# Performance work log

Hardware: AMD Instinct MI355X
Metric: run time of the kernel (lower is better)

## Reference

```python
import jax, jax.numpy as jnp
import numpy as np

N_NODES = 50000
N_EDGES = 1600000
DIM_IN = 64
DIM = 64
DIM_OUT = 32
N_GRAPHS = 64
DELTA = 2.5749
BN_EPS = 1e-5


def _lin(x, W, b):
    return x @ W.T + b


def _pna_conv(x, src, dst, mlp_W, mlp_b, W1, b1, W2, b2):
    # GINConv with overridden PNA aggregate: nn(x + aggr(x_j))
    msgs = x[src]                                               # [E, d]
    n = x.shape[0]
    sums = jax.ops.segment_sum(msgs, dst, num_segments=n)       # [N, d]
    maxs = jax.ops.segment_max(msgs, dst, num_segments=n)
    cnt = jax.ops.segment_sum(jnp.ones((msgs.shape[0], 1), msgs.dtype), dst,
                              num_segments=n)                   # [N, 1]
    means = sums / cnt
    var = jax.nn.relu(jax.ops.segment_sum(msgs * msgs, dst, num_segments=n) / cnt
                      - means * means)
    aggr = jnp.concatenate([sums, maxs, means, var], axis=1)    # [N, 4d]
    comb = jnp.concatenate([aggr, (cnt / DELTA) * aggr, (DELTA / cnt) * aggr],
                           axis=1)                              # [N, 12d]
    a = _lin(comb, mlp_W, mlp_b)                                # [N, d]
    h = x + a                                                   # (1+eps)*x + aggr, eps=0
    return _lin(jax.nn.relu(_lin(h, W1, b1)), W2, b2)


def _bn(x, g, b):
    # BatchNorm1d with batch statistics (training-mode stats, biased var)
    m = x.mean(axis=0)
    v = ((x - m) ** 2).mean(axis=0)
    return g * (x - m) / jnp.sqrt(v + BN_EPS) + b


def setup_inputs() -> dict:
    key = jax.random.key(0)
    ks = jax.random.split(key, 32)
    x = jax.random.normal(ks[0], (N_NODES, DIM_IN), dtype=jnp.float32)
    src = jax.random.randint(ks[1], (N_EDGES,), 0, N_NODES)
    dst = jax.random.randint(ks[2], (N_EDGES,), 0, N_NODES)
    # guarantee every node has >=1 incoming edge (original divides by bincount)
    dst = dst.at[:N_NODES].set(jnp.arange(N_NODES))
    edge_index = jnp.stack([src, dst]).astype(jnp.int32)
    batch = jnp.sort(jax.random.randint(ks[3], (N_NODES,), 0, N_GRAPHS)).astype(jnp.int32)

    def w(k, shape):
        return jax.random.normal(k, shape, dtype=jnp.float32) * 0.1

    d = {"x": x, "edge_index": edge_index, "batch": batch}
    i = 4
    for c in ("c1", "c2", "c3"):
        d[f"{c}_mlp_W"] = w(ks[i], (DIM, DIM * 12)); i += 1
        d[f"{c}_mlp_b"] = jnp.zeros((DIM,), jnp.float32)
        d[f"{c}_W1"] = w(ks[i], (DIM, DIM)); i += 1
        d[f"{c}_b1"] = jnp.zeros((DIM,), jnp.float32)
        d[f"{c}_W2"] = w(ks[i], (DIM, DIM)); i += 1
        d[f"{c}_b2"] = jnp.zeros((DIM,), jnp.float32)
    for b in ("bn1", "bn2", "bn3"):
        d[f"{b}_g"] = jnp.ones((DIM,), jnp.float32)
        d[f"{b}_b"] = jnp.zeros((DIM,), jnp.float32)
    d["fc1_W"] = w(ks[i], (DIM, DIM)); i += 1
    d["fc1_b"] = jnp.zeros((DIM,), jnp.float32)
    d["fc2_W"] = w(ks[i], (DIM_OUT, DIM)); i += 1
    d["fc2_b"] = jnp.zeros((DIM_OUT,), jnp.float32)
    return d


def reference(x, edge_index, batch,
              c1_mlp_W, c1_mlp_b, c1_W1, c1_b1, c1_W2, c1_b2, bn1_g, bn1_b,
              c2_mlp_W, c2_mlp_b, c2_W1, c2_b1, c2_W2, c2_b2, bn2_g, bn2_b,
              c3_mlp_W, c3_mlp_b, c3_W1, c3_b1, c3_W2, c3_b2, bn3_g, bn3_b,
              fc1_W, fc1_b, fc2_W, fc2_b):
    src, dst = edge_index[0], edge_index[1]
    h = jax.nn.relu(_pna_conv(x, src, dst, c1_mlp_W, c1_mlp_b, c1_W1, c1_b1, c1_W2, c1_b2))
    h = _bn(h, bn1_g, bn1_b)
    h = jax.nn.relu(_pna_conv(h, src, dst, c2_mlp_W, c2_mlp_b, c2_W1, c2_b1, c2_W2, c2_b2))
    h = _bn(h, bn2_g, bn2_b)
    h = jax.nn.relu(_pna_conv(h, src, dst, c3_mlp_W, c3_mlp_b, c3_W1, c3_b1, c3_W2, c3_b2))
    h = _bn(h, bn3_g, bn3_b)
    g = jax.ops.segment_sum(h, batch, num_segments=N_GRAPHS)   # global_add_pool
    g = jax.nn.relu(_lin(g, fc1_W, fc1_b))                     # dropout disabled (eval)
    g = _lin(g, fc2_W, fc2_b)
    return jax.nn.log_softmax(g, axis=-1)
```

## Files before the change

### kernel.cpp

```cpp
#include <hip/hip_runtime.h>

#define NN 50000
#define NE 1600000
#define DD 64
#define NGRAPH 64
#define DOUT 32
#define DELTA_F 2.5749f
#define BN_EPS_F 1e-5f

typedef unsigned short ushort;
typedef __attribute__((ext_vector_type(8))) short short8;
typedef __attribute__((ext_vector_type(4))) float floatx4;

static __device__ __forceinline__ float blo(unsigned u) {
    return __uint_as_float(u << 16);
}
static __device__ __forceinline__ float bhi(unsigned u) {
    return __uint_as_float(u & 0xFFFF0000u);
}
static __device__ __forceinline__ float bu2f(ushort u) {
    return __uint_as_float(((unsigned)u) << 16);
}
static __device__ __forceinline__ ushort f2bu(float f) {
    unsigned u = __float_as_uint(f);
    unsigned r = (u + 0x7FFF + ((u >> 16) & 1)) >> 16;
    return (ushort)r;
}
static __device__ __forceinline__ unsigned pk(float a, float b) {
    return ((unsigned)f2bu(b) << 16) | (unsigned)f2bu(a);
}

__global__ void k_prep(const float* __restrict__ x, ushort* __restrict__ XH,
                       const float* __restrict__ w0, const float* __restrict__ w1,
                       const float* __restrict__ w2,
                       const float* __restrict__ a0, const float* __restrict__ a1,
                       const float* __restrict__ a2, const float* __restrict__ a3,
                       const float* __restrict__ a4, const float* __restrict__ a5,
                       ushort* __restrict__ Wb, ushort* __restrict__ Wsb,
                       int* __restrict__ counts, float* __restrict__ bnstat,
                       float* __restrict__ gpool) {
    int i = blockIdx.x * 256 + threadIdx.x;
    if (i < NN) counts[i] = 0;
    if (i < 384) bnstat[i] = 0.f;
    if (i < NGRAPH * DD) gpool[i] = 0.f;
    if (i < NN * 16) {
        float4 v = *(const float4*)(x + (size_t)i * 4);
        ushort4 h;
        h.x = f2bu(v.x); h.y = f2bu(v.y); h.z = f2bu(v.z); h.w = f2bu(v.w);
        *(ushort4*)(XH + (size_t)i * 4) = h;
    }
    if (i < 3 * 65536) {
        int layer = i / 65536, r = i % 65536;
        const float* w = (layer == 0) ? w0 : ((layer == 1) ? w1 : w2);
        int c = r / 16384, r2 = r % 16384;
        int kb = r2 >> 11, r3 = r2 & 2047;
        int t = r3 >> 9, r4 = r3 & 511;
        int l = r4 >> 3, j = r4 & 7;
        int k = kb * 32 + (l >> 4) * 8 + j;
        int o = t * 16 + (l & 15);
        int g = (c == 0) ? 0 : ((c == 3) ? 2 : 1);
        float wv = w[o * 768 + g * 256 + k];
        ushort h = f2bu(wv);
        Wb[i] = (c == 2) ? f2bu(wv - bu2f(h)) : h;
    } else if (i < 3 * 65536 + 3 * 16384) {
        int i2 = i - 3 * 65536;
        int layer = i2 / 16384, r = i2 % 16384;
        int lin = r >> 13, r2 = r & 8191;
        int hl = r2 >> 12, r3 = r2 & 4095;
        int kb = r3 >> 11, r4 = r3 & 2047;
        int t = r4 >> 9, r5 = r4 & 511;
        int l = r5 >> 3, j = r5 & 7;
        int k = kb * 32 + (l >> 4) * 8 + j;
        int o = t * 16 + (l & 15);
        const float* w = (lin == 0)
            ? ((layer == 0) ? a0 : (layer == 1) ? a2 : a4)
            : ((layer == 0) ? a1 : (layer == 1) ? a3 : a5);
        float wv = w[o * 64 + k];
        ushort h = f2bu(wv);
        Wsb[i2] = hl ? f2bu(wv - bu2f(h)) : h;
    }
}

__global__ void k_rank(const int* __restrict__ dst, int* __restrict__ counts,
                       int* __restrict__ rank) {
    int i = blockIdx.x * 256 + threadIdx.x;
    if (i < NE / 4) {
        int4 d = ((const int4*)dst)[i];
        int4 r;
        r.x = atomicAdd(&counts[d.x], 1);
        r.y = atomicAdd(&counts[d.y], 1);
        r.z = atomicAdd(&counts[d.z], 1);
        r.w = atomicAdd(&counts[d.w], 1);
        ((int4*)rank)[i] = r;
    }
}

__global__ void k_scan_a(const int* __restrict__ counts, int* __restrict__ blockSums) {
    __shared__ int red[256];
    int tid = threadIdx.x;
    int gid = blockIdx.x * 256 + tid;
    int v = (gid < NN) ? counts[gid] : 0;
    red[tid] = v;
    __syncthreads();
    for (int s = 128; s > 0; s >>= 1) {
        if (tid < s) red[tid] += red[tid + s];
        __syncthreads();
    }
    if (tid == 0) blockSums[blockIdx.x] = red[0];
}

__global__ void k_scan_b(const int* __restrict__ blockSums, int* __restrict__ blockBase,
                         const int* __restrict__ batch, int* __restrict__ gcnt) {
    __shared__ int sh[256];
    int tid = threadIdx.x;
    int v = (tid < 196) ? blockSums[tid] : 0;
    sh[tid] = v;
    __syncthreads();
    for (int off = 1; off < 256; off <<= 1) {
        int t = (tid >= off) ? sh[tid - off] : 0;
        __syncthreads();
        sh[tid] += t;
        __syncthreads();
    }
    blockBase[tid] = sh[tid] - v;
    if (tid < NGRAPH) {
        auto lb = [&](int g) {
            int lo = 0, hi = NN;
            while (lo < hi) {
                int mid = (lo + hi) >> 1;
                if (batch[mid] < g) lo = mid + 1; else hi = mid;
            }
            return lo;
        };
        gcnt[tid] = lb(tid + 1) - lb(tid);
    }
}

__global__ void k_scan_c(const int* __restrict__ counts, const int* __restrict__ blockBase,
                         int* __restrict__ row_ptr) {
    __shared__ int sh[256];
    int tid = threadIdx.x;
    int gid = blockIdx.x * 256 + tid;
    int v = (gid < NN) ? counts[gid] : 0;
    sh[tid] = v;
    __syncthreads();
    for (int off = 1; off < 256; off <<= 1) {
        int t = (tid >= off) ? sh[tid - off] : 0;
        __syncthreads();
        sh[tid] += t;
        __syncthreads();
    }
    int excl = blockBase[blockIdx.x] + sh[tid] - v;
    if (gid <= NN) row_ptr[gid] = excl;
}

__global__ void k_place(const int* __restrict__ src, const int* __restrict__ dst,
                        const int* __restrict__ rank, const int* __restrict__ row_ptr,
                        int* __restrict__ csr_src) {
    int i = blockIdx.x * 256 + threadIdx.x;
    if (i < NE / 4) {
        int4 s4 = ((const int4*)src)[i];
        int4 d4 = ((const int4*)dst)[i];
        int4 r4 = ((const int4*)rank)[i];
        csr_src[row_ptr[d4.x] + r4.x] = s4.x;
        csr_src[row_ptr[d4.y] + r4.y] = s4.y;
        csr_src[row_ptr[d4.z] + r4.z] = s4.z;
        csr_src[row_ptr[d4.w] + r4.w] = s4.w;
    }
}

#define MBIAS(i) aux[i]
#define B1V(i)   aux[64 + (i)]
#define B2V(i)   aux[128 + (i)]
#define DEGV(m)  aux[192 + (m)]
#define AFFS(i)  aux[224 + (i)]
#define AFFB(i)  aux[288 + (i)]

__global__ __launch_bounds__(256, 4) void k_fused(
    const ushort* __restrict__ XHin, ushort* __restrict__ XHout,
    const int* __restrict__ row_ptr, const int* __restrict__ csr_src,
    const ushort* __restrict__ Wbh, const ushort* __restrict__ Wlin,
    const float* __restrict__ mlp_b,
    const float* __restrict__ b1, const float* __restrict__ b2,
    const float* __restrict__ affstat, const float* __restrict__ affg,
    const float* __restrict__ affb,
    float* __restrict__ bnstat,
    const int* __restrict__ batch, float* __restrict__ gpool, int do_pool) {
    __shared__ __align__(16) char smem[27136];
    ushort* const Agh = (ushort*)smem;
    ushort* const Agl = (ushort*)(smem + 12800);
    float* const aux = (float*)(smem + 25600);
    int* const ibatch = (int*)(smem + 27008);
    float* const hsf = (float*)smem;

    const int tid = threadIdx.x;
    const int node0 = blockIdx.x * 32;

    if (tid < 64) {
        MBIAS(tid) = mlp_b[tid];
        B1V(tid) = b1[tid];
        B2V(tid) = b2[tid];
        float A = 1.f, Bv = 0.f;
        if (affstat) {
            float mean = affstat[tid] * (1.f / NN);
            float var = fmaxf(affstat[64 + tid] * (1.f / NN) - mean * mean, 0.f);
            float inv = rsqrtf(var + BN_EPS_F);
            A = affg[tid] * inv;
            Bv = affb[tid] - mean * A;
        }
        AFFS(tid) = A;
        AFFB(tid) = Bv;
    }
    if (tid < 32) {
        int node = node0 + tid;
        ibatch[tid] = (do_pool && node < NN) ? batch[node] : -1;
    }
    __syncthreads();

    {
        const int l8 = tid & 7;
        const int m = tid >> 3;
        const int node = node0 + m;
        const int f0 = l8 * 8;
        const ushort* Xp = XHin + f0;

        float s[8], q[8], mx[8];
#pragma unroll
        for (int i = 0; i < 8; ++i) { s[i] = 0.f; q[i] = 0.f; mx[i] = -3.402823466e38f; }

        auto acc8 = [&](const uint4& rr) {
            float v0 = blo(rr.x), v1 = bhi(rr.x);
            float v2 = blo(rr.y), v3 = bhi(rr.y);
            float v4 = blo(rr.z), v5 = bhi(rr.z);
            float v6 = blo(rr.w), v7 = bhi(rr.w);
            s[0] += v0; q[0] = fmaf(v0, v0, q[0]); mx[0] = fmaxf(mx[0], v0);
            s[1] += v1; q[1] = fmaf(v1, v1, q[1]); mx[1] = fmaxf(mx[1], v1);
            s[2] += v2; q[2] = fmaf(v2, v2, q[2]); mx[2] = fmaxf(mx[2], v2);
            s[3] += v3; q[3] = fmaf(v3, v3, q[3]); mx[3] = fmaxf(mx[3], v3);
            s[4] += v4; q[4] = fmaf(v4, v4, q[4]); mx[4] = fmaxf(mx[4], v4);
            s[5] += v5; q[5] = fmaf(v5, v5, q[5]); mx[5] = fmaxf(mx[5], v5);
            s[6] += v6; q[6] = fmaf(v6, v6, q[6]); mx[6] = fmaxf(mx[6], v6);
            s[7] += v7; q[7] = fmaf(v7, v7, q[7]); mx[7] = fmaxf(mx[7], v7);
        };

        int beg = 0, end = 0;
        if (node < NN) { beg = row_ptr[node]; end = row_ptr[node + 1]; }
        const int deg = end - beg;
        const int nb = (deg + 3) >> 2;

        uint4 ra[4], rb[4];
        int ia[4];
        if (nb > 0) {
#pragma unroll
            for (int j = 0; j < 4; ++j) {
                int e = beg + j;
                ia[j] = csr_src[(e < end) ? e : end - 1];
            }
#pragma unroll
            for (int j = 0; j < 4; ++j)
                ra[j] = *(const uint4*)(Xp + (size_t)ia[j] * 64);
            if (nb > 1) {
#pragma unroll
                for (int j = 0; j < 4; ++j) {
                    int e = beg + 4 + j;
                    ia[j] = csr_src[(e < end) ? e : end - 1];
                }
            }
        }
        for (int t = 0; t < nb; ++t) {
            if (t + 1 < nb) {
#pragma unroll
                for (int j = 0; j < 4; ++j)
                    rb[j] = *(const uint4*)(Xp + (size_t)ia[j] * 64);
            }
            if (t + 2 < nb) {
                int b2e = beg + (t + 2) * 4;
#pragma unroll
                for (int j = 0; j < 4; ++j) {
                    int e = b2e + j;
                    ia[j] = csr_src[(e < end) ? e : end - 1];
                }
            }
            int cnt = end - (beg + t * 4);
            if (cnt >= 4) {
#pragma unroll
                for (int j = 0; j < 4; ++j) acc8(ra[j]);
            } else {
#pragma unroll
                for (int j = 0; j < 4; ++j) if (j < cnt) acc8(ra[j]);
            }
            if (t + 1 < nb) {
#pragma unroll
                for (int j = 0; j < 4; ++j) ra[j] = rb[j];
            }
        }

        float cdeg = (node < NN) ? (float)deg : 1.f;
        float rc = 1.0f / cdeg;
        float var[8];
#pragma unroll
        for (int i = 0; i < 8; ++i) {
            float mean = s[i] * rc;
            var[i] = fmaxf(q[i] * rc - mean * mean, 0.f);
            if (node >= NN) { mx[i] = 0.f; var[i] = 0.f; }
        }
#pragma unroll
        for (int i = 0; i < 8; ++i) {
            float Af = AFFS(f0 + i), Bf = AFFB(f0 + i);
            s[i] = Af * s[i] + cdeg * Bf;
            mx[i] = Af * mx[i] + Bf;
            var[i] = Af * Af * var[i];
        }
        ushort* dh = Agh + m * 200 + f0;
        ushort* dl = Agl + m * 200 + f0;
        auto emit8 = [&](const float* v, int off) {
            ushort h0 = f2bu(v[0]), h1 = f2bu(v[1]), h2 = f2bu(v[2]), h3 = f2bu(v[3]);
            ushort h4 = f2bu(v[4]), h5 = f2bu(v[5]), h6 = f2bu(v[6]), h7 = f2bu(v[7]);
            uint4 hv;
            hv.x = (unsigned)h0 | ((unsigned)h1 << 16);
            hv.y = (unsigned)h2 | ((unsigned)h3 << 16);
            hv.z = (unsigned)h4 | ((unsigned)h5 << 16);
            hv.w = (unsigned)h6 | ((unsigned)h7 << 16);
            uint4 lv;
            lv.x = pk(v[0] - bu2f(h0), v[1] - bu2f(h1));
            lv.y = pk(v[2] - bu2f(h2), v[3] - bu2f(h3));
            lv.z = pk(v[4] - bu2f(h4), v[5] - bu2f(h5));
            lv.w = pk(v[6] - bu2f(h6), v[7] - bu2f(h7));
            *(uint4*)(dh + off) = hv;
            *(uint4*)(dl + off) = lv;
        };
        emit8(s, 0);
        emit8(mx, 64);
        emit8(var, 128);
        if (l8 == 0) DEGV(m) = cdeg;
    }
    __syncthreads();

    const int ln = tid & 63, wvi = tid >> 6;
    const int quad = ln >> 4, l16 = ln & 15;
    const int mtile = wvi >> 1;
    const int nt0 = (wvi & 1) * 2;

    const ushort* ArowH = Agh + (mtile * 16 + l16) * 200 + quad * 8;
    const ushort* ArowL = Agl + (mtile * 16 + l16) * 200 + quad * 8;
    short8 afh[6];
#pragma unroll
    for (int i = 0; i < 6; ++i) {
        const int off = (i >> 1) * 64 + (i & 1) * 32;
        afh[i] = *(const short8*)(ArowH + off);
    }
    __syncthreads();

#pragma unroll
    for (int nti = 0; nti < 2; ++nti) {
        const int nt = nt0 + nti;
        floatx4 aA0 = (floatx4){0.f, 0.f, 0.f, 0.f};
        floatx4 aB0 = (floatx4){0.f, 0.f, 0.f, 0.f};
        floatx4 aA1 = (floatx4){0.f, 0.f, 0.f, 0.f};
        floatx4 aB1 = (floatx4){0.f, 0.f, 0.f, 0.f};
        floatx4 aA2 = (floatx4){0.f, 0.f, 0.f, 0.f};
        floatx4 aB2 = (floatx4){0.f, 0.f, 0.f, 0.f};
#pragma unroll
        for (int kb = 0; kb < 8; ++kb) {
            const int am = (kb < 4) ? kb : ((kb < 6) ? (kb - 4) : (kb - 2));
            const int base = ((kb * 4 + nt) * 512) + ln * 8;
            short8 w0 = *(const short8*)(Wbh + base);
            short8 w1h = *(const short8*)(Wbh + 16384 + base);
            short8 w2 = *(const short8*)(Wbh + 3 * 16384 + base);
            if (kb == 4 || kb == 5) {
                aB0 = __builtin_amdgcn_mfma_f32_16x16x32_bf16(afh[am], w0, aB0, 0, 0, 0);
                aB1 = __builtin_amdgcn_mfma_f32_16x16x32_bf16(afh[am], w1h, aB1, 0, 0, 0);
                aB2 = __builtin_amdgcn_mfma_f32_16x16x32_bf16(afh[am], w2, aB2, 0, 0, 0);
            } else {
                short8 w1l = *(const short8*)(Wbh + 2 * 16384 + base);
                short8 al = *(const short8*)(ArowL + ((am >> 1) * 64 + (am & 1) * 32));
                aA0 = __builtin_amdgcn_mfma_f32_16x16x32_bf16(afh[am], w0, aA0, 0, 0, 0);
                aA1 = __builtin_amdgcn_mfma_f32_16x16x32_bf16(afh[am], w1h, aA1, 0, 0, 0);
                aA1 = __builtin_amdgcn_mfma_f32_16x16x32_bf16(al, w1h, aA1, 0, 0, 0);
                aA1 = __builtin_amdgcn_mfma_f32_16x16x32_bf16(afh[am], w1l, aA1, 0, 0, 0);
                aA2 = __builtin_amdgcn_mfma_f32_16x16x32_bf16(afh[am], w2, aA2, 0, 0, 0);
            }
        }
#pragma unroll
        for (int r = 0; r < 4; ++r) {
            int m = mtile * 16 + quad * 4 + r;
            float dg = DEGV(m), rcd = 1.f / dg;
            float cA2 = DELTA_F * rcd;
            float cB2 = DELTA_F * rcd * rcd;
            float cA1 = dg * (1.0f / DELTA_F);
            int n = nt * 16 + l16;
            hsf[n * 34 + m] = aA0[r] + rcd * aB0[r]
                            + cA2 * aA2[r] + cB2 * aB2[r]
                            + cA1 * aA1[r] + (1.0f / DELTA_F) * aB1[r];
        }
    }
    __syncthreads();

    const int tx = tid & 15, ty = tid >> 4;
    const int o0 = tx * 4, n0 = ty * 2;
#pragma unroll
    for (int ni = 0; ni < 2; ++ni) {
        int n = n0 + ni;
        int node = node0 + n;
        float xa4[4] = {0.f, 0.f, 0.f, 0.f};
        if (node < NN) {
            ushort4 hx = *(const ushort4*)(XHin + (size_t)node * DD + o0);
            xa4[0] = AFFS(o0 + 0) * bu2f(hx.x) + AFFB(o0 + 0);
            xa4[1] = AFFS(o0 + 1) * bu2f(hx.y) + AFFB(o0 + 1);
            xa4[2] = AFFS(o0 + 2) * bu2f(hx.z) + AFFB(o0 + 2);
            xa4[3] = AFFS(o0 + 3) * bu2f(hx.w) + AFFB(o0 + 3);
        }
#pragma unroll
        for (int oi = 0; oi < 4; ++oi) {
            int idx = (o0 + oi) * 34 + n;
            hsf[idx] = hsf[idx] + xa4[oi] + MBIAS(o0 + oi);
        }
    }
    __syncthreads();

    {
        floatx4 lacc[2];
        lacc[0] = (floatx4){0.f, 0.f, 0.f, 0.f};
        lacc[1] = (floatx4){0.f, 0.f, 0.f, 0.f};
#pragma unroll
        for (int kb = 0; kb < 2; ++kb) {
            short8 ah, al;
#pragma unroll
            for (int j = 0; j < 8; ++j) {
                float v = hsf[(kb * 32 + quad * 8 + j) * 34 + mtile * 16 + l16];
                ushort h = f2bu(v);
                ah[j] = (short)h;
                al[j] = (short)f2bu(v - bu2f(h));
            }
#pragma unroll
            for (int nti = 0; nti < 2; ++nti) {
                const int boff = ((kb * 4 + nt0 + nti) * 512) + ln * 8;
                short8 wh = *(const short8*)(Wlin + boff);
                short8 wl = *(const short8*)(Wlin + 4096 + boff);
                lacc[nti] = __builtin_amdgcn_mfma_f32_16x16x32_bf16(ah, wh, lacc[nti], 0, 0, 0);
                lacc[nti] = __builtin_amdgcn_mfma_f32_16x16x32_bf16(al, wh, lacc[nti], 0, 0, 0);
                lacc[nti] = __builtin_amdgcn_mfma_f32_16x16x32_bf16(ah, wl, lacc[nti], 0, 0, 0);
            }
        }
        __syncthreads();
#pragma unroll
        for (int nti = 0; nti < 2; ++nti) {
            int o = (nt0 + nti) * 16 + l16;
#pragma unroll
            for (int r = 0; r < 4; ++r)
                hsf[o * 34 + mtile * 16 + quad * 4 + r] = fmaxf(lacc[nti][r] + B1V(o), 0.f);
        }
    }
    __syncthreads();

    {
        floatx4 lacc[2];
        lacc[0] = (floatx4){0.f, 0.f, 0.f, 0.f};
        lacc[1] = (floatx4){0.f, 0.f, 0.f, 0.f};
#pragma unroll
        for (int kb = 0; kb < 2; ++kb) {
            short8 ah, al;
#pragma unroll
            for (int j = 0; j < 8; ++j) {
                float v = hsf[(kb * 32 + quad * 8 + j) * 34 + mtile * 16 + l16];
                ushort h = f2bu(v);
                ah[j] = (short)h;
                al[j] = (short)f2bu(v - bu2f(h));
            }
#pragma unroll
            for (int nti = 0; nti < 2; ++nti) {
                const int boff = ((kb * 4 + nt0 + nti) * 512) + ln * 8;
                short8 wh = *(const short8*)(Wlin + 8192 + boff);
                short8 wl = *(const short8*)(Wlin + 12288 + boff);
                lacc[nti] = __builtin_amdgcn_mfma_f32_16x16x32_bf16(ah, wh, lacc[nti], 0, 0, 0);
                lacc[nti] = __builtin_amdgcn_mfma_f32_16x16x32_bf16(al, wh, lacc[nti], 0, 0, 0);
                lacc[nti] = __builtin_amdgcn_mfma_f32_16x16x32_bf16(ah, wl, lacc[nti], 0, 0, 0);
            }
        }
        __syncthreads();
#pragma unroll
        for (int nti = 0; nti < 2; ++nti) {
            int o = (nt0 + nti) * 16 + l16;
#pragma unroll
            for (int r = 0; r < 4; ++r)
                hsf[o * 34 + mtile * 16 + quad * 4 + r] = fmaxf(lacc[nti][r] + B2V(o), 0.f);
        }
    }
    __syncthreads();

    if (XHout) {
#pragma unroll
        for (int ni = 0; ni < 2; ++ni) {
            int n = n0 + ni;
            int node = node0 + n;
            if (node < NN) {
                ushort4 h;
                h.x = f2bu(hsf[(o0 + 0) * 34 + n]);
                h.y = f2bu(hsf[(o0 + 1) * 34 + n]);
                h.z = f2bu(hsf[(o0 + 2) * 34 + n]);
                h.w = f2bu(hsf[(o0 + 3) * 34 + n]);
                *(ushort4*)(XHout + (size_t)node * DD + o0) = h;
            }
        }
    }

    if (tid < 64) {
        float s = 0.f, sq = 0.f;
        float pacc = 0.f;
        int curg = ibatch[0];
        int lim = NN - node0;
        if (lim > 32) lim = 32;
        for (int n = 0; n < lim; ++n) {
            float v = hsf[tid * 34 + n];
            s += v;
            sq += v * v;
            if (do_pool) {
                int g = ibatch[n];
                if (g != curg) {
                    atomicAdd(&gpool[(size_t)curg * DD + tid], pacc);
                    pacc = 0.f;
                    curg = g;
                }
                pacc += v;
            }
        }
        if (do_pool && curg >= 0)
            atomicAdd(&gpool[(size_t)curg * DD + tid], pacc);
        atomicAdd(&bnstat[tid], s);
        atomicAdd(&bnstat[64 + tid], sq);
    }
}

__global__ __launch_bounds__(256) void k_head(const float* __restrict__ gpool,
                                              const float* __restrict__ bs3,
                                              const float* __restrict__ g3,
                                              const float* __restrict__ b3,
                                              const int* __restrict__ gcnt,
                                              const float* __restrict__ fc1W, const float* __restrict__ fc1b,
                                              const float* __restrict__ fc2W, const float* __restrict__ fc2b,
                                              float* __restrict__ out) {
    __shared__ float sh[12640];
    float* const gs = sh;
    float* const w1t = sh + 4096;
    float* const z1s = sh + 8256;
    float* const b1s = sh + 12416;
    float* const b2s = sh + 12480;
    float* const sc3 = sh + 12512;
    float* const shf3 = sh + 12576;
    float* const w2t = sh;
    float* const z2s = sh + 4096;

    int tid = threadIdx.x;
    if (tid < 64) {
        float mean = bs3[tid] * (1.f / NN);
        float var = fmaxf(bs3[64 + tid] * (1.f / NN) - mean * mean, 0.f);
        float inv = rsqrtf(var + BN_EPS_F);
        float A = g3[tid] * inv;
        sc3[tid] = A;
        shf3[tid] = b3[tid] - mean * A;
    }
    __syncthreads();
    for (int i = tid; i < 4096; i += 256) {
        int o = i >> 6, j = i & 63;
        gs[i] = sc3[j] * gpool[i] + shf3[j] * (float)gcnt[o];
        w1t[j * 65 + o] = fc1W[i];
    }
    if (tid < 64) b1s[tid] = fc1b[tid];
    if (tid < 32) b2s[tid] = fc2b[tid];
    __syncthreads();
    {
        int tx = tid & 15, ty = tid >> 4, o0 = tx * 4, g0 = ty * 4;
        float acc[16];
#pragma unroll
        for (int i = 0; i < 16; ++i) acc[i] = 0.f;
        for (int j = 0; j < 64; ++j) {
            float w0 = w1t[j * 65 + o0 + 0], w1 = w1t[j * 65 + o0 + 1];
            float w2 = w1t[j * 65 + o0 + 2], w3 = w1t[j * 65 + o0 + 3];
#pragma unroll
            for (int gi = 0; gi < 4; ++gi) {
                float a = gs[(g0 + gi) * 64 + j];
                acc[gi * 4 + 0] += a * w0; acc[gi * 4 + 1] += a * w1;
                acc[gi * 4 + 2] += a * w2; acc[gi * 4 + 3] += a * w3;
            }
        }
        __syncthreads();
#pragma unroll
        for (int gi = 0; gi < 4; ++gi)
#pragma unroll
            for (int oi = 0; oi < 4; ++oi)
                z1s[(g0 + gi) * 65 + o0 + oi] = fmaxf(acc[gi * 4 + oi] + b1s[o0 + oi], 0.f);
    }
    for (int i = tid; i < 2048; i += 256) {
        int o = i >> 6, j = i & 63;
        w2t[j * 33 + o] = fc2W[i];
    }
    __syncthreads();
    {
        int tx = tid & 7, ty = tid >> 3, o0 = tx * 4, g0 = ty * 2;
        float acc[8];
#pragma unroll
        for (int i = 0; i < 8; ++i) acc[i] = 0.f;
        for (int j = 0; j < 64; ++j) {
            float w0 = w2t[j * 33 + o0 + 0], w1 = w2t[j * 33 + o0 + 1];
            float w2 = w2t[j * 33 + o0 + 2], w3 = w2t[j * 33 + o0 + 3];
            float a0 = z1s[(g0 + 0) * 65 + j];
            float a1 = z1s[(g0 + 1) * 65 + j];
            acc[0] += a0 * w0; acc[1] += a0 * w1; acc[2] += a0 * w2; acc[3] += a0 * w3;
            acc[4] += a1 * w0; acc[5] += a1 * w1; acc[6] += a1 * w2; acc[7] += a1 * w3;
        }
#pragma unroll
        for (int gi = 0; gi < 2; ++gi)
#pragma unroll
            for (int oi = 0; oi < 4; ++oi)
                z2s[(g0 + gi) * 33 + o0 + oi] = acc[gi * 4 + oi] + b2s[o0 + oi];
    }
    __syncthreads();
    if (tid < 64) {
        float m = -3.402823466e38f;
        for (int c = 0; c < DOUT; ++c) m = fmaxf(m, z2s[tid * 33 + c]);
        float s = 0.f;
        for (int c = 0; c < DOUT; ++c) s += expf(z2s[tid * 33 + c] - m);
        float lse = m + logf(s);
        for (int c = 0; c < DOUT; ++c)
            out[tid * DOUT + c] = z2s[tid * 33 + c] - lse;
    }
}

extern "C" void kernel_launch(void* const* d_in, const int* in_sizes, int n_in,
                              void* d_out, int out_size, void* d_ws, size_t ws_size,
                              hipStream_t stream) {
    const float* x = (const float*)d_in[0];
    const int* ei = (const int*)d_in[1];
    const int* src = ei;
    const int* dst = ei + NE;
    const int* batch = (const int*)d_in[2];
    const float *mlpW[3], *mlpB[3], *w1[3], *bb1[3], *w2[3], *bb2[3], *bng[3], *bnb[3];
    for (int l = 0; l < 3; ++l) {
        mlpW[l] = (const float*)d_in[3 + 6 * l];
        mlpB[l] = (const float*)d_in[4 + 6 * l];
        w1[l]   = (const float*)d_in[5 + 6 * l];
        bb1[l]  = (const float*)d_in[6 + 6 * l];
        w2[l]   = (const float*)d_in[7 + 6 * l];
        bb2[l]  = (const float*)d_in[8 + 6 * l];
        bng[l]  = (const float*)d_in[21 + 2 * l];
        bnb[l]  = (const float*)d_in[22 + 2 * l];
    }
    const float* fc1W = (const float*)d_in[27];
    const float* fc1b = (const float*)d_in[28];
    const float* fc2W = (const float*)d_in[29];
    const float* fc2b = (const float*)d_in[30];
    float* out = (float*)d_out;

    char* ws = (char*)d_ws;
    size_t off = 0;
    auto alloc = [&](size_t bytes) -> void* {
        void* p = ws + off;
        off = (off + bytes + 511) & ~(size_t)511;
        return p;
    };
    int* counts    = (int*)alloc((size_t)NN * 4);
    int* row_ptr   = (int*)alloc((size_t)(NN + 1) * 4);
    int* rank      = (int*)alloc((size_t)NE * 4);
    int* blockSums = (int*)alloc(256 * 4);
    int* blockBase = (int*)alloc(256 * 4);
    int* csr_src   = (int*)alloc((size_t)NE * 4);
    ushort* XHA    = (ushort*)alloc((size_t)NN * DD * 2);
    ushort* XHB    = (ushort*)alloc((size_t)NN * DD * 2);
    ushort* Wb     = (ushort*)alloc((size_t)3 * 65536 * 2);
    ushort* Wsb    = (ushort*)alloc((size_t)3 * 16384 * 2);
    float* bnstat  = (float*)alloc(384 * 4);
    float* gpool   = (float*)alloc((size_t)NGRAPH * DD * 4);
    int* gcnt      = (int*)alloc(NGRAPH * 4);
    (void)ws_size; (void)in_sizes; (void)n_in; (void)out_size;

    k_prep<<<3125, 256, 0, stream>>>(x, XHA,
                                     mlpW[0], mlpW[1], mlpW[2],
                                     w1[0], w2[0], w1[1], w2[1], w1[2], w2[2],
                                     Wb, Wsb, counts, bnstat, gpool);
    k_rank<<<1563, 256, 0, stream>>>(dst, counts, rank);
    k_scan_a<<<196, 256, 0, stream>>>(counts, blockSums);
    k_scan_b<<<1, 256, 0, stream>>>(blockSums, blockBase, batch, gcnt);
    k_scan_c<<<196, 256, 0, stream>>>(counts, blockBase, row_ptr);
    k_place<<<1563, 256, 0, stream>>>(src, dst, rank, row_ptr, csr_src);

    k_fused<<<1563, 256, 0, stream>>>(XHA, XHB, row_ptr, csr_src,
                                      Wb, Wsb, mlpB[0], bb1[0], bb2[0],
                                      nullptr, nullptr, nullptr,
                                      bnstat, batch, gpool, 0);
    k_fused<<<1563, 256, 0, stream>>>(XHB, XHA, row_ptr, csr_src,
                                      Wb + 65536, Wsb + 16384, mlpB[1], bb1[1], bb2[1],
                                      bnstat, bng[0], bnb[0],
                                      bnstat + 128, batch, gpool, 0);
    k_fused<<<1563, 256, 0, stream>>>(XHA, nullptr, row_ptr, csr_src,
                                      Wb + 2 * 65536, Wsb + 2 * 16384, mlpB[2], bb1[2], bb2[2],
                                      bnstat + 128, bng[1], bnb[1],
                                      bnstat + 256, batch, gpool, 1);
    k_head<<<1, 256, 0, stream>>>(gpool, bnstat + 256, bng[2], bnb[2], gcnt,
                                  fc1W, fc1b, fc2W, fc2b, out);
}
```

Before: 458.1 us.

## Sort nodes by in-degree to balance gather work in fused conv kernels

Adds a counting sort of nodes by in-degree (histogram, scan, place) and has each fused conv block process a permuted set of 32 nodes with similar degree. The goal is less intra-block imbalance in the edge-gather loop, where one high-degree node would otherwise stall its block. Because permuted blocks no longer hold contiguous nodes of the same graph, global pooling moves out of the last conv into a separate pooling kernel that writes and rereads the layer-3 output. The cost is three small preprocessing launches, scattered node reads and writes, and an extra pass over the output.

```diff
diff --git a/kernel.cpp b/kernel.cpp
--- a/kernel.cpp
+++ b/kernel.cpp
@@ -169,6 +169,58 @@
     }
 }
 
+__global__ void k_dhist(const int* __restrict__ row_ptr, int* __restrict__ BH) {
+    __shared__ int h[256];
+    int tid = threadIdx.x;
+    h[tid] = 0;
+    __syncthreads();
+    int gid = blockIdx.x * 256 + tid;
+    if (gid < NN) {
+        int d = row_ptr[gid + 1] - row_ptr[gid];
+        if (d > 255) d = 255;
+        atomicAdd(&h[d], 1);
+    }
+    __syncthreads();
+    BH[blockIdx.x * 256 + tid] = h[tid];
+}
+
+__global__ void k_dscan(int* __restrict__ BH) {
+    __shared__ int sh[256];
+    int b = threadIdx.x;
+    int run = 0;
+    for (int blk = 0; blk < 196; ++blk) {
+        int t = BH[blk * 256 + b];
+        BH[blk * 256 + b] = run;
+        run += t;
+    }
+    sh[b] = run;
+    __syncthreads();
+    for (int off = 1; off < 256; off <<= 1) {
+        int t = (b >= off) ? sh[b - off] : 0;
+        __syncthreads();
+        sh[b] += t;
+        __syncthreads();
+    }
+    int base = sh[b] - run;
+    for (int blk = 0; blk < 196; ++blk)
+        BH[blk * 256 + b] += base;
+}
+
+__global__ void k_dplace(const int* __restrict__ row_ptr, const int* __restrict__ BH,
+                         int* __restrict__ perm) {
+    __shared__ int h[256];
+    int tid = threadIdx.x;
+    h[tid] = 0;
+    __syncthreads();
+    int gid = blockIdx.x * 256 + tid;
+    if (gid < NN) {
+        int d = row_ptr[gid + 1] - row_ptr[gid];
+        if (d > 255) d = 255;
+        int lr = atomicAdd(&h[d], 1);
+        perm[BH[blockIdx.x * 256 + d] + lr] = gid;
+    }
+}
+
 #define MBIAS(i) aux[i]
 #define B1V(i)   aux[64 + (i)]
 #define B2V(i)   aux[128 + (i)]
@@ -178,19 +230,19 @@
 
 __global__ __launch_bounds__(256, 4) void k_fused(
     const ushort* __restrict__ XHin, ushort* __restrict__ XHout,
+    const int* __restrict__ perm,
     const int* __restrict__ row_ptr, const int* __restrict__ csr_src,
     const ushort* __restrict__ Wbh, const ushort* __restrict__ Wlin,
     const float* __restrict__ mlp_b,
     const float* __restrict__ b1, const float* __restrict__ b2,
     const float* __restrict__ affstat, const float* __restrict__ affg,
     const float* __restrict__ affb,
-    float* __restrict__ bnstat,
-    const int* __restrict__ batch, float* __restrict__ gpool, int do_pool) {
+    float* __restrict__ bnstat) {
     __shared__ __align__(16) char smem[27136];
     ushort* const Agh = (ushort*)smem;
     ushort* const Agl = (ushort*)(smem + 12800);
     float* const aux = (float*)(smem + 25600);
-    int* const ibatch = (int*)(smem + 27008);
+    int* const pnod = (int*)(smem + 27008);
     float* const hsf = (float*)smem;
 
     const int tid = threadIdx.x;
@@ -212,15 +264,15 @@
         AFFB(tid) = Bv;
     }
     if (tid < 32) {
-        int node = node0 + tid;
-        ibatch[tid] = (do_pool && node < NN) ? batch[node] : -1;
+        int sl = node0 + tid;
+        pnod[tid] = (sl < NN) ? perm[sl] : -1;
     }
     __syncthreads();
 
     {
         const int l8 = tid & 7;
         const int m = tid >> 3;
-        const int node = node0 + m;
+        const int node = pnod[m];
         const int f0 = l8 * 8;
         const ushort* Xp = XHin + f0;
 
@@ -244,7 +296,7 @@
         };
 
         int beg = 0, end = 0;
-        if (node < NN) { beg = row_ptr[node]; end = row_ptr[node + 1]; }
+        if (node >= 0) { beg = row_ptr[node]; end = row_ptr[node + 1]; }
         const int deg = end - beg;
         const int nb = (deg + 3) >> 2;
 
@@ -295,14 +347,14 @@
             }
         }
 
-        float cdeg = (node < NN) ? (float)deg : 1.f;
+        float cdeg = (node >= 0) ? (float)deg : 1.f;
         float rc = 1.0f / cdeg;
         float var[8];
 #pragma unroll
         for (int i = 0; i < 8; ++i) {
             float mean = s[i] * rc;
             var[i] = fmaxf(q[i] * rc - mean * mean, 0.f);
-            if (node >= NN) { mx[i] = 0.f; var[i] = 0.f; }
+            if (node < 0) { mx[i] = 0.f; var[i] = 0.f; }
         }
 #pragma unroll
         for (int i = 0; i < 8; ++i) {
@@ -401,9 +453,9 @@
 #pragma unroll
     for (int ni = 0; ni < 2; ++ni) {
         int n = n0 + ni;
-        int node = node0 + n;
+        int node = pnod[n];
         float xa4[4] = {0.f, 0.f, 0.f, 0.f};
-        if (node < NN) {
+        if (node >= 0) {
             ushort4 hx = *(const ushort4*)(XHin + (size_t)node * DD + o0);
             xa4[0] = AFFS(o0 + 0) * bu2f(hx.x) + AFFB(o0 + 0);
             xa4[1] = AFFS(o0 + 1) * bu2f(hx.y) + AFFB(o0 + 1);
@@ -492,8 +544,8 @@
 #pragma unroll
         for (int ni = 0; ni < 2; ++ni) {
             int n = n0 + ni;
-            int node = node0 + n;
-            if (node < NN) {
+            int node = pnod[n];
+            if (node >= 0) {
                 ushort4 h;
                 h.x = f2bu(hsf[(o0 + 0) * 34 + n]);
                 h.y = f2bu(hsf[(o0 + 1) * 34 + n]);
@@ -506,28 +558,57 @@
 
     if (tid < 64) {
         float s = 0.f, sq = 0.f;
-        float pacc = 0.f;
-        int curg = ibatch[0];
         int lim = NN - node0;
         if (lim > 32) lim = 32;
         for (int n = 0; n < lim; ++n) {
             float v = hsf[tid * 34 + n];
             s += v;
             sq += v * v;
-            if (do_pool) {
-                int g = ibatch[n];
-                if (g != curg) {
-                    atomicAdd(&gpool[(size_t)curg * DD + tid], pacc);
-                    pacc = 0.f;
-                    curg = g;
-                }
-                pacc += v;
-            }
-        }
-        if (do_pool && curg >= 0)
-            atomicAdd(&gpool[(size_t)curg * DD + tid], pacc);
+        }
         atomicAdd(&bnstat[tid], s);
         atomicAdd(&bnstat[64 + tid], sq);
+    }
+}
+
+__global__ __launch_bounds__(256) void k_pool3(
+    const ushort* __restrict__ YH, const int* __restrict__ batch,
+    float* __restrict__ gpool) {
+    __shared__ float pool[512];
+    int tid = threadIdx.x;
+    int i = blockIdx.x * 256 + tid;
+    int n = i >> 4, fq = (i & 15) * 4;
+    float4 r = make_float4(0.f, 0.f, 0.f, 0.f);
+    bool valid = i < NN * 16;
+    if (valid) {
+        ushort4 h = *(const ushort4*)(YH + (size_t)n * DD + fq);
+        r.x = bu2f(h.x); r.y = bu2f(h.y); r.z = bu2f(h.z); r.w = bu2f(h.w);
+    }
+    int nfirst = blockIdx.x * 16;
+    int nlast = nfirst + 15;
+    if (nlast >= NN) nlast = NN - 1;
+    int gmin = batch[nfirst], gmax = batch[nlast];
+    int span = gmax - gmin + 1;
+    if (span <= 8) {
+        for (int j = tid; j < span * 64; j += 256) pool[j] = 0.f;
+        __syncthreads();
+        if (valid) {
+            int gb = batch[n] - gmin;
+            atomicAdd(&pool[gb * 64 + fq + 0], r.x);
+            atomicAdd(&pool[gb * 64 + fq + 1], r.y);
+            atomicAdd(&pool[gb * 64 + fq + 2], r.z);
+            atomicAdd(&pool[gb * 64 + fq + 3], r.w);
+        }
+        __syncthreads();
+        for (int j = tid; j < span * 64; j += 256)
+            atomicAdd(&gpool[(size_t)(gmin + (j >> 6)) * 64 + (j & 63)], pool[j]);
+    } else {
+        if (valid) {
+            float* gp = gpool + (size_t)batch[n] * DD + fq;
+            atomicAdd(gp + 0, r.x);
+            atomicAdd(gp + 1, r.y);
+            atomicAdd(gp + 2, r.z);
+            atomicAdd(gp + 3, r.w);
+        }
     }
 }
 
@@ -664,6 +745,8 @@
     int* blockSums = (int*)alloc(256 * 4);
     int* blockBase = (int*)alloc(256 * 4);
     int* csr_src   = (int*)alloc((size_t)NE * 4);
+    int* blockHist = (int*)alloc((size_t)196 * 256 * 4);
+    int* perm      = (int*)alloc((size_t)NN * 4);
     ushort* XHA    = (ushort*)alloc((size_t)NN * DD * 2);
     ushort* XHB    = (ushort*)alloc((size_t)NN * DD * 2);
     ushort* Wb     = (ushort*)alloc((size_t)3 * 65536 * 2);
@@ -682,19 +765,23 @@
     k_scan_b<<<1, 256, 0, stream>>>(blockSums, blockBase, batch, gcnt);
     k_scan_c<<<196, 256, 0, stream>>>(counts, blockBase, row_ptr);
     k_place<<<1563, 256, 0, stream>>>(src, dst, rank, row_ptr, csr_src);
-
-    k_fused<<<1563, 256, 0, stream>>>(XHA, XHB, row_ptr, csr_src,
+    k_dhist<<<196, 256, 0, stream>>>(row_ptr, blockHist);
+    k_dscan<<<1, 256, 0, stream>>>(blockHist);
+    k_dplace<<<196, 256, 0, stream>>>(row_ptr, blockHist, perm);
+
+    k_fused<<<1563, 256, 0, stream>>>(XHA, XHB, perm, row_ptr, csr_src,
                                       Wb, Wsb, mlpB[0], bb1[0], bb2[0],
                                       nullptr, nullptr, nullptr,
-                                      bnstat, batch, gpool, 0);
-    k_fused<<<1563, 256, 0, stream>>>(XHB, XHA, row_ptr, csr_src,
+                                      bnstat);
+    k_fused<<<1563, 256, 0, stream>>>(XHB, XHA, perm, row_ptr, csr_src,
                                       Wb + 65536, Wsb + 16384, mlpB[1], bb1[1], bb2[1],
                                       bnstat, bng[0], bnb[0],
-                                      bnstat + 128, batch, gpool, 0);
-    k_fused<<<1563, 256, 0, stream>>>(XHA, nullptr, row_ptr, csr_src,
+                                      bnstat + 128);
+    k_fused<<<1563, 256, 0, stream>>>(XHA, XHB, perm, row_ptr, csr_src,
                                       Wb + 2 * 65536, Wsb + 2 * 16384, mlpB[2], bb1[2], bb2[2],
                                       bnstat + 128, bng[1], bnb[1],
-                                      bnstat + 256, batch, gpool, 1);
+                                      bnstat + 256);
+    k_pool3<<<3125, 256, 0, stream>>>(XHB, batch, gpool);
     k_head<<<1, 256, 0, stream>>>(gpool, bnstat + 256, bng[2], bnb[2], gcnt,
                                   fc1W, fc1b, fc2W, fc2b, out);
 }
```

After: 488.3 us. 1.07x slower.

## Sort nodes by in-degree so fused blocks process similar-degree nodes together

Applied to the files above, without the earlier changes.

Builds a per-block degree histogram during the scan, prefix-sums it across blocks, and produces a permutation that orders nodes by in-degree (clamped at 255). The fused conv kernels for the first two layers index nodes through this permutation, so each block's 32 nodes have similar degree, which reduces wavefront divergence in the edge-aggregation loop. The third layer keeps natural order, which preserves the contiguous batch runs that the pooling code relies on. The cost is an extra histogram pass, a permutation lookup, and node row reads and writes that become scattered instead of contiguous.

```diff
diff --git a/kernel.cpp b/kernel.cpp
--- a/kernel.cpp
+++ b/kernel.cpp
@@ -95,54 +95,83 @@
     }
 }
 
-__global__ void k_scan_a(const int* __restrict__ counts, int* __restrict__ blockSums) {
+__global__ void k_scan_a(const int* __restrict__ counts, int* __restrict__ blockSums,
+                         int* __restrict__ BH) {
     __shared__ int red[256];
+    __shared__ int h[256];
     int tid = threadIdx.x;
+    h[tid] = 0;
     int gid = blockIdx.x * 256 + tid;
     int v = (gid < NN) ? counts[gid] : 0;
     red[tid] = v;
     __syncthreads();
+    if (gid < NN) {
+        int d = (v > 255) ? 255 : v;
+        atomicAdd(&h[d], 1);
+    }
     for (int s = 128; s > 0; s >>= 1) {
         if (tid < s) red[tid] += red[tid + s];
         __syncthreads();
     }
     if (tid == 0) blockSums[blockIdx.x] = red[0];
-}
-
-__global__ void k_scan_b(const int* __restrict__ blockSums, int* __restrict__ blockBase,
+    BH[blockIdx.x * 256 + tid] = h[tid];
+}
+
+__global__ void k_scanB2(int* __restrict__ BH, int* __restrict__ binTot,
+                         const int* __restrict__ blockSums, int* __restrict__ blockBase,
                          const int* __restrict__ batch, int* __restrict__ gcnt) {
     __shared__ int sh[256];
-    int tid = threadIdx.x;
-    int v = (tid < 196) ? blockSums[tid] : 0;
-    sh[tid] = v;
-    __syncthreads();
-    for (int off = 1; off < 256; off <<= 1) {
-        int t = (tid >= off) ? sh[tid - off] : 0;
-        __syncthreads();
-        sh[tid] += t;
-        __syncthreads();
-    }
-    blockBase[tid] = sh[tid] - v;
-    if (tid < NGRAPH) {
-        auto lb = [&](int g) {
-            int lo = 0, hi = NN;
-            while (lo < hi) {
-                int mid = (lo + hi) >> 1;
-                if (batch[mid] < g) lo = mid + 1; else hi = mid;
-            }
-            return lo;
-        };
-        gcnt[tid] = lb(tid + 1) - lb(tid);
-    }
-}
-
-__global__ void k_scan_c(const int* __restrict__ counts, const int* __restrict__ blockBase,
-                         int* __restrict__ row_ptr) {
+    int t = threadIdx.x;
+    if (blockIdx.x < 256) {
+        int b = blockIdx.x;
+        int v = (t < 196) ? BH[t * 256 + b] : 0;
+        sh[t] = v;
+        __syncthreads();
+        for (int off = 1; off < 256; off <<= 1) {
+            int tv = (t >= off) ? sh[t - off] : 0;
+            __syncthreads();
+            sh[t] += tv;
+            __syncthreads();
+        }
+        if (t < 196) BH[t * 256 + b] = sh[t] - v;
+        if (t == 255) binTot[b] = sh[255];
+    } else {
+        int v = (t < 196) ? blockSums[t] : 0;
+        sh[t] = v;
+        __syncthreads();
+        for (int off = 1; off < 256; off <<= 1) {
+            int tv = (t >= off) ? sh[t - off] : 0;
+            __syncthreads();
+            sh[t] += tv;
+            __syncthreads();
+        }
+        blockBase[t] = sh[t] - v;
+        if (t < NGRAPH) {
+            auto lb = [&](int g) {
+                int lo = 0, hi = NN;
+                while (lo < hi) {
+                    int mid = (lo + hi) >> 1;
+                    if (batch[mid] < g) lo = mid + 1; else hi = mid;
+                }
+                return lo;
+            };
+            gcnt[t] = lb(t + 1) - lb(t);
+        }
+    }
+}
+
+__global__ void k_scanC2(const int* __restrict__ counts, const int* __restrict__ blockBase,
+                         int* __restrict__ row_ptr,
+                         const int* __restrict__ BH, const int* __restrict__ binTot,
+                         int* __restrict__ perm) {
     __shared__ int sh[256];
+    __shared__ int h2[256];
+    __shared__ int bb[256];
     int tid = threadIdx.x;
     int gid = blockIdx.x * 256 + tid;
     int v = (gid < NN) ? counts[gid] : 0;
     sh[tid] = v;
+    h2[tid] = 0;
     __syncthreads();
     for (int off = 1; off < 256; off <<= 1) {
         int t = (tid >= off) ? sh[tid - off] : 0;
@@ -152,6 +181,23 @@
     }
     int excl = blockBase[blockIdx.x] + sh[tid] - v;
     if (gid <= NN) row_ptr[gid] = excl;
+    __syncthreads();
+    int bt = binTot[tid];
+    sh[tid] = bt;
+    __syncthreads();
+    for (int off = 1; off < 256; off <<= 1) {
+        int t = (tid >= off) ? sh[tid - off] : 0;
+        __syncthreads();
+        sh[tid] += t;
+        __syncthreads();
+    }
+    bb[tid] = (sh[tid] - bt) + BH[blockIdx.x * 256 + tid];
+    __syncthreads();
+    if (gid < NN) {
+        int d = (v > 255) ? 255 : v;
+        int lr = atomicAdd(&h2[d], 1);
+        perm[bb[d] + lr] = gid;
+    }
 }
 
 __global__ void k_place(const int* __restrict__ src, const int* __restrict__ dst,
@@ -178,6 +224,7 @@
 
 __global__ __launch_bounds__(256, 4) void k_fused(
     const ushort* __restrict__ XHin, ushort* __restrict__ XHout,
+    const int* __restrict__ perm,
     const int* __restrict__ row_ptr, const int* __restrict__ csr_src,
     const ushort* __restrict__ Wbh, const ushort* __restrict__ Wlin,
     const float* __restrict__ mlp_b,
@@ -186,11 +233,12 @@
     const float* __restrict__ affb,
     float* __restrict__ bnstat,
     const int* __restrict__ batch, float* __restrict__ gpool, int do_pool) {
-    __shared__ __align__(16) char smem[27136];
+    __shared__ __align__(16) char smem[27264];
     ushort* const Agh = (ushort*)smem;
     ushort* const Agl = (ushort*)(smem + 12800);
     float* const aux = (float*)(smem + 25600);
-    int* const ibatch = (int*)(smem + 27008);
+    int* const pnod = (int*)(smem + 27008);
+    int* const ibatch = (int*)(smem + 27136);
     float* const hsf = (float*)smem;
 
     const int tid = threadIdx.x;
@@ -212,15 +260,17 @@
         AFFB(tid) = Bv;
     }
     if (tid < 32) {
-        int node = node0 + tid;
-        ibatch[tid] = (do_pool && node < NN) ? batch[node] : -1;
+        int sl = node0 + tid;
+        int nd = (sl < NN) ? (perm ? perm[sl] : sl) : -1;
+        pnod[tid] = nd;
+        ibatch[tid] = (do_pool && nd >= 0) ? batch[nd] : -1;
     }
     __syncthreads();
 
     {
         const int l8 = tid & 7;
         const int m = tid >> 3;
-        const int node = node0 + m;
+        const int node = pnod[m];
         const int f0 = l8 * 8;
         const ushort* Xp = XHin + f0;
 
@@ -244,7 +294,7 @@
         };
 
         int beg = 0, end = 0;
-        if (node < NN) { beg = row_ptr[node]; end = row_ptr[node + 1]; }
+        if (node >= 0) { beg = row_ptr[node]; end = row_ptr[node + 1]; }
         const int deg = end - beg;
         const int nb = (deg + 3) >> 2;
 
@@ -295,14 +345,14 @@
             }
         }
 
-        float cdeg = (node < NN) ? (float)deg : 1.f;
+        float cdeg = (node >= 0) ? (float)deg : 1.f;
         float rc = 1.0f / cdeg;
         float var[8];
 #pragma unroll
         for (int i = 0; i < 8; ++i) {
             float mean = s[i] * rc;
             var[i] = fmaxf(q[i] * rc - mean * mean, 0.f);
-            if (node >= NN) { mx[i] = 0.f; var[i] = 0.f; }
+            if (node < 0) { mx[i] = 0.f; var[i] = 0.f; }
         }
 #pragma unroll
         for (int i = 0; i < 8; ++i) {
@@ -401,9 +451,9 @@
 #pragma unroll
     for (int ni = 0; ni < 2; ++ni) {
         int n = n0 + ni;
-        int node = node0 + n;
+        int node = pnod[n];
         float xa4[4] = {0.f, 0.f, 0.f, 0.f};
-        if (node < NN) {
+        if (node >= 0) {
             ushort4 hx = *(const ushort4*)(XHin + (size_t)node * DD + o0);
             xa4[0] = AFFS(o0 + 0) * bu2f(hx.x) + AFFB(o0 + 0);
             xa4[1] = AFFS(o0 + 1) * bu2f(hx.y) + AFFB(o0 + 1);
@@ -492,8 +542,8 @@
 #pragma unroll
         for (int ni = 0; ni < 2; ++ni) {
             int n = n0 + ni;
-            int node = node0 + n;
-            if (node < NN) {
+            int node = pnod[n];
+            if (node >= 0) {
                 ushort4 h;
                 h.x = f2bu(hsf[(o0 + 0) * 34 + n]);
                 h.y = f2bu(hsf[(o0 + 1) * 34 + n]);
@@ -664,6 +714,9 @@
     int* blockSums = (int*)alloc(256 * 4);
     int* blockBase = (int*)alloc(256 * 4);
     int* csr_src   = (int*)alloc((size_t)NE * 4);
+    int* blockHist = (int*)alloc((size_t)196 * 256 * 4);
+    int* binTot    = (int*)alloc(256 * 4);
+    int* perm      = (int*)alloc((size_t)NN * 4);
     ushort* XHA    = (ushort*)alloc((size_t)NN * DD * 2);
     ushort* XHB    = (ushort*)alloc((size_t)NN * DD * 2);
     ushort* Wb     = (ushort*)alloc((size_t)3 * 65536 * 2);
@@ -678,20 +731,20 @@
                                      w1[0], w2[0], w1[1], w2[1], w1[2], w2[2],
                                      Wb, Wsb, counts, bnstat, gpool);
     k_rank<<<1563, 256, 0, stream>>>(dst, counts, rank);
-    k_scan_a<<<196, 256, 0, stream>>>(counts, blockSums);
-    k_scan_b<<<1, 256, 0, stream>>>(blockSums, blockBase, batch, gcnt);
-    k_scan_c<<<196, 256, 0, stream>>>(counts, blockBase, row_ptr);
+    k_scan_a<<<196, 256, 0, stream>>>(counts, blockSums, blockHist);
+    k_scanB2<<<257, 256, 0, stream>>>(blockHist, binTot, blockSums, blockBase, batch, gcnt);
+    k_scanC2<<<196, 256, 0, stream>>>(counts, blockBase, row_ptr, blockHist, binTot, perm);
     k_place<<<1563, 256, 0, stream>>>(src, dst, rank, row_ptr, csr_src);
 
-    k_fused<<<1563, 256, 0, stream>>>(XHA, XHB, row_ptr, csr_src,
+    k_fused<<<1563, 256, 0, stream>>>(XHA, XHB, perm, row_ptr, csr_src,
                                       Wb, Wsb, mlpB[0], bb1[0], bb2[0],
                                       nullptr, nullptr, nullptr,
                                       bnstat, batch, gpool, 0);
-    k_fused<<<1563, 256, 0, stream>>>(XHB, XHA, row_ptr, csr_src,
+    k_fused<<<1563, 256, 0, stream>>>(XHB, XHA, perm, row_ptr, csr_src,
                                       Wb + 65536, Wsb + 16384, mlpB[1], bb1[1], bb2[1],
                                       bnstat, bng[0], bnb[0],
                                       bnstat + 128, batch, gpool, 0);
-    k_fused<<<1563, 256, 0, stream>>>(XHA, nullptr, row_ptr, csr_src,
+    k_fused<<<1563, 256, 0, stream>>>(XHA, nullptr, nullptr, row_ptr, csr_src,
                                       Wb + 2 * 65536, Wsb + 2 * 16384, mlpB[2], bb1[2], bb2[2],
                                       bnstat + 128, bng[1], bnb[1],
                                       bnstat + 256, batch, gpool, 1);
```

Measured after the change: 454.9 us. Within noise of the previous version (-0.7%).
